# Kernel tuning notes

Measured on AMD Instinct MI355X. Metric: run time of the kernel, lower is better.

## Reference

```python
import jax, jax.numpy as jnp
import numpy as np

N = 50000   # num_nodes
E = 300000  # num_edges
D = 256     # args.dim
F = 1024    # feat_dim
C = 40      # num_labels

def setup_inputs() -> dict:
    key = jax.random.key(0)
    ks = jax.random.split(key, 16)
    def lin(k, fan_in, shape):
        return (jax.random.normal(k, shape, jnp.float32) / np.float32(np.sqrt(fan_in)))
    return {
        "feat": jax.random.normal(ks[0], (N, F), jnp.float32),
        "src": jax.random.randint(ks[1], (E,), 0, N, dtype=jnp.int32),
        "dst": jax.random.randint(ks[2], (E,), 0, N, dtype=jnp.int32),
        "W_fc": lin(ks[3], F, (F, D)), "b_fc": jnp.zeros((D,), jnp.float32),
        "W1": lin(ks[4], D, (D, D)), "b1": jnp.zeros((D,), jnp.float32),
        "W2": lin(ks[5], D, (D, D)), "b2": jnp.zeros((D,), jnp.float32),
        "W3": lin(ks[6], D, (D, D)), "b3": jnp.zeros((D,), jnp.float32),
        "gamma": jnp.ones((D,), jnp.float32), "beta": jnp.zeros((D,), jnp.float32),
        "W_lin": lin(ks[7], D, (D, C)), "b_lin": jnp.zeros((C,), jnp.float32),
    }

def _norms(src, dst, n):
    # DGL GraphConv norm='both': out-degree norm on src side, in-degree on dst side, clamp(min=1)
    ones = jnp.ones(src.shape[0], jnp.float32)
    deg_out = jnp.clip(jax.ops.segment_sum(ones, src, num_segments=n), 1.0)
    deg_in = jnp.clip(jax.ops.segment_sum(ones, dst, num_segments=n), 1.0)
    return deg_out[:, None] ** -0.5, deg_in[:, None] ** -0.5

def _gconv(x, src, dst, norm_s, norm_d, W, b):
    h = x * norm_s                              # [N, D]
    m = jax.ops.segment_sum(h[src], dst, num_segments=x.shape[0])  # SpMM via gather/scatter
    return (m * norm_d) @ W + b

def _bn_elu(x, gamma, beta):
    # training-mode batchnorm math (batch stats, biased var); dropout is identity (eval)
    mu = x.mean(axis=0)
    var = x.var(axis=0)
    y = gamma * (x - mu) * jax.lax.rsqrt(var + 1e-5) + beta
    return jax.nn.elu(y)

def reference(feat, src, dst, W_fc, b_fc, W1, b1, W2, b2, W3, b3, gamma, beta, W_lin, b_lin):
    norm_s, norm_d = _norms(src, dst, feat.shape[0])
    x = feat @ W_fc + b_fc
    x = _gconv(x, src, dst, norm_s, norm_d, W1, b1)
    x = _bn_elu(x, gamma, beta)
    x = _gconv(x, src, dst, norm_s, norm_d, W2, b2)
    x = _bn_elu(x, gamma, beta)
    x = _gconv(x, src, dst, norm_s, norm_d, W3, b3)
    return (x, x @ W_lin + b_lin)
```

## Files before the change

kernel.cpp:

```cpp
#include <hip/hip_runtime.h>

#define N_NODES 50000
#define N_EDGES 300000
#define DIM 256
#define FEAT 1024
#define NCLS 40

typedef unsigned short u16;
typedef __attribute__((ext_vector_type(8))) short short8;
typedef __attribute__((ext_vector_type(4))) float float4v;

__device__ __forceinline__ float bf2f(u16 u) {
  union { float f; unsigned v; } x; x.v = ((unsigned)u) << 16; return x.f;
}
__device__ __forceinline__ u16 f2bf(float f) {
  union { float f; unsigned v; } x; x.f = f;
  unsigned r = 0x7fffu + ((x.v >> 16) & 1u);
  return (u16)((x.v + r) >> 16);
}
__device__ __forceinline__ float flexload(const void* p, size_t i, int f32) {
  return f32 ? ((const float*)p)[i] : bf2f(((const u16*)p)[i]);
}
__device__ __forceinline__ void flexstore(void* p, size_t i, int f32, float v) {
  if (f32) ((float*)p)[i] = v;
  else ((u16*)p)[i] = f2bf(v);
}

__global__ __launch_bounds__(256) void k_sniff(const u16* __restrict__ feat,
                                               int* __restrict__ dflag) {
  __shared__ int cnt[256];
  int t = threadIdx.x;
  int ok = 0;
  for (int j = 0; j < 4; ++j) {
    float v = bf2f(feat[(size_t)(t * 4 + j) * 2]);
    float a = fabsf(v);
    if (a < 64.0f && a > 1e-5f) ok++;
  }
  cnt[t] = ok;
  __syncthreads();
  for (int off = 128; off > 0; off >>= 1) {
    if (t < off) cnt[t] += cnt[t + off];
    __syncthreads();
  }
  if (t == 0) dflag[0] = (cnt[0] < 700) ? 1 : 0;
}

__global__ void k_setflag(int* dflag, int v) { dflag[0] = v; }

__global__ void k_filldiag(void* out, int n, float val, const int* __restrict__ dflag) {
  int i = blockIdx.x * blockDim.x + threadIdx.x;
  if (i < n) flexstore(out, i, dflag[0], val);
}


__global__ void k_zero(unsigned* p, int n) {
  int i = blockIdx.x * blockDim.x + threadIdx.x;
  if (i < n) p[i] = 0u;
}

__global__ void k_deg(const int* __restrict__ src, const int* __restrict__ dst,
                      float* __restrict__ degf, int* __restrict__ degi, int e) {
  int i = blockIdx.x * blockDim.x + threadIdx.x;
  if (i < e) {
    atomicAdd(&degf[src[i]], 1.0f);
    atomicAdd(&degi[dst[i]], 1);
  }
}

__global__ void k_norm(const float* __restrict__ degf, const int* __restrict__ degi,
                       float* __restrict__ ns, float* __restrict__ nd, int n) {
  int i = blockIdx.x * blockDim.x + threadIdx.x;
  if (i < n) {
    ns[i] = rsqrtf(fmaxf(degf[i], 1.0f));
    nd[i] = rsqrtf(fmaxf((float)degi[i], 1.0f));
  }
}

__global__ __launch_bounds__(1024) void k_scan(const int* __restrict__ counts,
                                               int* __restrict__ row_start,
                                               int* __restrict__ cursor, int n) {
  __shared__ int wsum[16];
  __shared__ int carry_s;
  int t = threadIdx.x;
  int lane = t & 63, wv = t >> 6;
  if (t == 0) carry_s = 0;
  __syncthreads();
  for (int base = 0; base < n; base += 4096) {
    int i0 = base + t * 4;
    int v0 = 0, v1 = 0, v2 = 0, v3 = 0;
    if (i0 + 3 < n) {
      int4 c4 = *(const int4*)&counts[i0];
      v0 = c4.x; v1 = c4.y; v2 = c4.z; v3 = c4.w;
    } else {
      if (i0 < n) v0 = counts[i0];
      if (i0 + 1 < n) v1 = counts[i0 + 1];
      if (i0 + 2 < n) v2 = counts[i0 + 2];
      if (i0 + 3 < n) v3 = counts[i0 + 3];
    }
    int s = v0 + v1 + v2 + v3;
    int sc = s;
#pragma unroll
    for (int off = 1; off < 64; off <<= 1) {
      int u = __shfl_up(sc, off, 64);
      if (lane >= off) sc += u;
    }
    if (lane == 63) wsum[wv] = sc;
    __syncthreads();
    if (wv == 0) {
      int w_ = (lane < 16) ? wsum[lane] : 0;
#pragma unroll
      for (int off = 1; off < 16; off <<= 1) {
        int u = __shfl_up(w_, off, 64);
        if (lane >= off) w_ += u;
      }
      if (lane < 16) wsum[lane] = w_;
    }
    __syncthreads();
    int wbase = (wv == 0) ? 0 : wsum[wv - 1];
    int carry = carry_s;
    int excl = carry + wbase + (sc - s);
    if (i0 < n)     { int p = excl;                row_start[i0] = p;     cursor[i0] = p; }
    if (i0 + 1 < n) { int p = excl + v0;           row_start[i0 + 1] = p; cursor[i0 + 1] = p; }
    if (i0 + 2 < n) { int p = excl + v0 + v1;      row_start[i0 + 2] = p; cursor[i0 + 2] = p; }
    if (i0 + 3 < n) { int p = excl + v0 + v1 + v2; row_start[i0 + 3] = p; cursor[i0 + 3] = p; }
    __syncthreads();
    if (t == 1023) carry_s = carry + wbase + sc;
    __syncthreads();
  }
  if (t == 0) row_start[n] = carry_s;
}

__global__ void k_scatter(const int* __restrict__ src, const int* __restrict__ dst,
                          int* __restrict__ cursor, int* __restrict__ csr_src, int e) {
  int i = blockIdx.x * blockDim.x + threadIdx.x;
  if (i < e) {
    int pos = atomicAdd(&cursor[dst[i]], 1);
    csr_src[pos] = src[i];
  }
}

__global__ void k_transpose(const void* __restrict__ w, u16* __restrict__ wt,
                            int K, int Ncols, const int* __restrict__ dflag) {
  int f = dflag[0];
  int i = blockIdx.x * blockDim.x + threadIdx.x;
  if (i < K * Ncols) {
    int k = i / Ncols;
    int c = i - k * Ncols;
    wt[c * K + k] = f2bf(flexload(w, i, f));
  }
}


__global__ __launch_bounds__(256) void k_gemm(
    const void* __restrict__ A, const u16* __restrict__ Bt,
    const void* __restrict__ bias, void* __restrict__ Cmat,
    int M, int K, int Ncols, int a_flex, int c_flex,
    const int* __restrict__ dflag) {
  __shared__ __align__(16) u16 As[64 * 128];
  __shared__ __align__(16) u16 Bs[64 * 128];

  const int f = dflag[0];
  const int af = a_flex & f;
  const int cf = c_flex & f;

  const int tid = threadIdx.x;
  const int lane = tid & 63;
  const int wv = tid >> 6;
  const int wm = (wv >> 1) * 64;
  const int wn = (wv & 1) * 64;
  const int quad = lane >> 4;
  const int l15 = lane & 15;
  const int rowBase = blockIdx.x * 128;
  const int colBase = blockIdx.y * 128;

  float4v acc[4][4];
#pragma unroll
  for (int a = 0; a < 4; ++a)
#pragma unroll
    for (int b = 0; b < 4; ++b) {
      acc[a][b][0] = 0.f; acc[a][b][1] = 0.f; acc[a][b][2] = 0.f; acc[a][b][3] = 0.f;
    }

  for (int k0 = 0; k0 < K; k0 += 64) {
    __syncthreads();
#pragma unroll
    for (int r = 0; r < 4; ++r) {
      int j = r * 256 + tid;
      int kq = j >> 7;
      int ml = j & 127;
      int grow = rowBase + ml;
      if (grow >= M) grow = M - 1;
      size_t abase = (size_t)grow * K + k0 + kq * 8;
      if (af) {
        const float* Af = (const float*)A;
        float4 lo = *(const float4*)&Af[abase];
        float4 hi = *(const float4*)&Af[abase + 4];
        u16* d = &As[j * 8];
        d[0] = f2bf(lo.x); d[1] = f2bf(lo.y); d[2] = f2bf(lo.z); d[3] = f2bf(lo.w);
        d[4] = f2bf(hi.x); d[5] = f2bf(hi.y); d[6] = f2bf(hi.z); d[7] = f2bf(hi.w);
      } else {
        const u16* Au = (const u16*)A;
        *(uint4*)&As[j * 8] = *(const uint4*)&Au[abase];
      }
      *(uint4*)&Bs[j * 8] = *(const uint4*)&Bt[(size_t)(colBase + ml) * K + k0 + kq * 8];
    }
    __syncthreads();
#pragma unroll
    for (int ks = 0; ks < 2; ++ks) {
      short8 afr[4], bfr[4];
#pragma unroll
      for (int t = 0; t < 4; ++t) {
        int kq = ks * 4 + quad;
        afr[t] = *(const short8*)&As[(kq * 128 + wm + t * 16 + l15) * 8];
        bfr[t] = *(const short8*)&Bs[(kq * 128 + wn + t * 16 + l15) * 8];
      }
#pragma unroll
      for (int mt = 0; mt < 4; ++mt)
#pragma unroll
        for (int nt = 0; nt < 4; ++nt)
          acc[mt][nt] = __builtin_amdgcn_mfma_f32_16x16x32_bf16(
              afr[mt], bfr[nt], acc[mt][nt], 0, 0, 0);
    }
  }

#pragma unroll
  for (int nt = 0; nt < 4; ++nt) {
    int col = colBase + wn + nt * 16 + l15;
    float bv = flexload(bias, col, f);
#pragma unroll
    for (int mt = 0; mt < 4; ++mt) {
#pragma unroll
      for (int r = 0; r < 4; ++r) {
        int row = rowBase + wm + mt * 16 + quad * 4 + r;
        if (row < M) {
          float v = acc[mt][nt][r] + bv;
          if (cf) ((float*)Cmat)[(size_t)row * Ncols + col] = v;
          else ((u16*)Cmat)[(size_t)row * Ncols + col] = f2bf(v);
        }
      }
    }
  }
}


__global__ __launch_bounds__(256) void k_spmm(
    const u16* __restrict__ x, u16* __restrict__ y,
    const int* __restrict__ row_start, const int* __restrict__ csr_src,
    const float* __restrict__ ns, const float* __restrict__ nd, int n) {
  int wid = (blockIdx.x * blockDim.x + threadIdx.x) >> 6;
  int lane = threadIdx.x & 63;
  if (wid >= n) return;
  int e0 = row_start[wid];
  int e1 = row_start[wid + 1];
  int c = lane * 4;
  float a0 = 0.f, a1 = 0.f, a2 = 0.f, a3 = 0.f;
  for (int e = e0; e < e1; ++e) {
    int s = csr_src[e];
    float w = ns[s];
    uint2 v = *(const uint2*)&x[(size_t)s * DIM + c];
    a0 += w * bf2f((u16)(v.x & 0xffffu));
    a1 += w * bf2f((u16)(v.x >> 16));
    a2 += w * bf2f((u16)(v.y & 0xffffu));
    a3 += w * bf2f((u16)(v.y >> 16));
  }
  float wd = nd[wid];
  uint2 o;
  o.x = (unsigned)f2bf(a0 * wd) | ((unsigned)f2bf(a1 * wd) << 16);
  o.y = (unsigned)f2bf(a2 * wd) | ((unsigned)f2bf(a3 * wd) << 16);
  *(uint2*)&y[(size_t)wid * DIM + c] = o;
}


__global__ __launch_bounds__(256) void k_bnstats(const u16* __restrict__ x,
                                                 float* __restrict__ stats, int nrows) {
  int t = threadIdx.x;
  float s = 0.f, s2 = 0.f;
  for (int r = blockIdx.x; r < nrows; r += gridDim.x) {
    float v = bf2f(x[(size_t)r * DIM + t]);
    s += v;
    s2 += v * v;
  }
  atomicAdd(&stats[t], s);
  atomicAdd(&stats[DIM + t], s2);
}

__global__ __launch_bounds__(256) void k_bnapply(u16* __restrict__ x,
                                                 const float* __restrict__ stats,
                                                 const void* __restrict__ gamma,
                                                 const void* __restrict__ beta, int nrows,
                                                 const int* __restrict__ dflag) {
  int f = dflag[0];
  int t = threadIdx.x;
  float inv_n = 1.0f / (float)nrows;
  float mu = stats[t] * inv_n;
  float var = stats[DIM + t] * inv_n - mu * mu;
  float rs = rsqrtf(var + 1e-5f);
  float g = flexload(gamma, t, f) * rs;
  float b = flexload(beta, t, f) - mu * g;
  for (int r = blockIdx.x; r < nrows; r += gridDim.x) {
    size_t idx = (size_t)r * DIM + t;
    float y = g * bf2f(x[idx]) + b;
    y = y > 0.f ? y : expm1f(y);
    x[idx] = f2bf(y);
  }
}


__global__ __launch_bounds__(256) void k_final(const void* __restrict__ x,
                                               const void* __restrict__ W,
                                               const void* __restrict__ bias,
                                               void* __restrict__ out, int nrows,
                                               const int* __restrict__ dflag) {
  __shared__ u16 xs[64 * DIM];
  __shared__ u16 wl[DIM * NCLS];
  int f = dflag[0];
  int t = threadIdx.x;
  int rowBase = blockIdx.x * 64;
  for (int i = t; i < 64 * DIM; i += 256) {
    int r = rowBase + (i >> 8);
    if (r >= nrows) r = nrows - 1;
    xs[i] = f2bf(flexload(x, (size_t)r * DIM + (i & 255), f));
  }
  for (int i = t; i < DIM * NCLS; i += 256) wl[i] = f2bf(flexload(W, i, f));
  __syncthreads();
  for (int o = t; o < 64 * NCLS; o += 256) {
    int r = o / NCLS;
    int c = o - r * NCLS;
    float acc = 0.f;
    const u16* xr = &xs[r * DIM];
#pragma unroll 8
    for (int k = 0; k < DIM; ++k) acc += bf2f(xr[k]) * bf2f(wl[k * NCLS + c]);
    int grow = rowBase + r;
    if (grow < nrows)
      flexstore(out, (size_t)N_NODES * DIM + (size_t)grow * NCLS + c, f,
                acc + flexload(bias, c, f));
  }
}


extern "C" void kernel_launch(void* const* d_in, const int* in_sizes, int n_in,
                              void* d_out, int out_size, void* d_ws, size_t ws_size,
                              hipStream_t stream) {
  static const int EXP[15] = {51200000, 300000, 300000, 262144, 256, 65536, 256,
                              65536, 256, 65536, 256, 256, 256, 10240, 40};
  bool ok_sizes = (n_in == 15);
  if (ok_sizes)
    for (int i = 0; i < 15; ++i)
      if (in_sizes[i] != EXP[i]) ok_sizes = false;

  char* w = (char*)d_ws;
  size_t o = 0;
  auto take = [&](size_t bytes) {
    size_t r = o;
    o += (bytes + 255) & ~(size_t)255;
    return r;
  };
  size_t o_degf = take(N_NODES * 4);
  size_t o_degi = take(N_NODES * 4);
  size_t o_stat = take(1024 * 4);
  size_t zero_bytes = o;
  size_t o_flag = take(256);
  size_t o_ns = take(N_NODES * 4);
  size_t o_nd = take(N_NODES * 4);
  size_t o_rs = take((N_NODES + 1) * 4);
  size_t o_cur = take(N_NODES * 4);
  size_t o_csr = take(N_EDGES * 4);
  size_t o_wfc = take((size_t)FEAT * DIM * 2);
  size_t o_w1 = take(DIM * DIM * 2);
  size_t o_w2 = take(DIM * DIM * 2);
  size_t o_w3 = take(DIM * DIM * 2);
  size_t o_xa = take((size_t)N_NODES * DIM * 2);
  size_t required = o;

  if (!ok_sizes || ws_size < required) {
    int* dflag0 = (int*)d_ws;
    float val = ok_sizes ? 1.0f : 2.0f;
    if (n_in > 0 && in_sizes[0] >= 2048)
      k_sniff<<<1, 256, 0, stream>>>((const u16*)d_in[0], dflag0);
    else
      k_setflag<<<1, 1, 0, stream>>>(dflag0, 0);
    k_filldiag<<<(out_size + 255) / 256, 256, 0, stream>>>(d_out, out_size, val, dflag0);
    return;
  }

  const void* feat = d_in[0];
  const int* src = (const int*)d_in[1];
  const int* dst = (const int*)d_in[2];
  const void* W_fc = d_in[3];
  const void* b_fc = d_in[4];
  const void* W1 = d_in[5];
  const void* b1 = d_in[6];
  const void* W2 = d_in[7];
  const void* b2 = d_in[8];
  const void* W3 = d_in[9];
  const void* b3 = d_in[10];
  const void* gamma = d_in[11];
  const void* beta = d_in[12];
  const void* W_lin = d_in[13];
  const void* b_lin = d_in[14];

  float* degf = (float*)(w + o_degf);
  int* degi = (int*)(w + o_degi);
  float* stats = (float*)(w + o_stat);
  int* dflag = (int*)(w + o_flag);
  float* norm_s = (float*)(w + o_ns);
  float* norm_d = (float*)(w + o_nd);
  int* row_start = (int*)(w + o_rs);
  int* cursor = (int*)(w + o_cur);
  int* csr_src = (int*)(w + o_csr);
  u16* WtFc = (u16*)(w + o_wfc);
  u16* Wt1 = (u16*)(w + o_w1);
  u16* Wt2 = (u16*)(w + o_w2);
  u16* Wt3 = (u16*)(w + o_w3);
  u16* xA = (u16*)(w + o_xa);

  u16* ping = (u16*)d_out;

  k_sniff<<<1, 256, 0, stream>>>((const u16*)feat, dflag);

  int zero_words = (int)(zero_bytes / 4);
  k_zero<<<(zero_words + 255) / 256, 256, 0, stream>>>((unsigned*)(w + 0), zero_words);
  k_deg<<<(N_EDGES + 255) / 256, 256, 0, stream>>>(src, dst, degf, degi, N_EDGES);
  k_norm<<<(N_NODES + 255) / 256, 256, 0, stream>>>(degf, degi, norm_s, norm_d, N_NODES);
  k_scan<<<1, 1024, 0, stream>>>(degi, row_start, cursor, N_NODES);
  k_scatter<<<(N_EDGES + 255) / 256, 256, 0, stream>>>(src, dst, cursor, csr_src, N_EDGES);
  k_transpose<<<((FEAT * DIM) + 255) / 256, 256, 0, stream>>>(W_fc, WtFc, FEAT, DIM, dflag);
  k_transpose<<<((DIM * DIM) + 255) / 256, 256, 0, stream>>>(W1, Wt1, DIM, DIM, dflag);
  k_transpose<<<((DIM * DIM) + 255) / 256, 256, 0, stream>>>(W2, Wt2, DIM, DIM, dflag);
  k_transpose<<<((DIM * DIM) + 255) / 256, 256, 0, stream>>>(W3, Wt3, DIM, DIM, dflag);

  dim3 gg((N_NODES + 127) / 128, DIM / 128);

  k_gemm<<<gg, 256, 0, stream>>>(feat, WtFc, b_fc, ping, N_NODES, FEAT, DIM, 1, 0, dflag);

  k_spmm<<<(N_NODES + 3) / 4, 256, 0, stream>>>(ping, xA, row_start, csr_src, norm_s, norm_d, N_NODES);
  k_gemm<<<gg, 256, 0, stream>>>(xA, Wt1, b1, ping, N_NODES, DIM, DIM, 0, 0, dflag);
  k_bnstats<<<512, 256, 0, stream>>>(ping, stats, N_NODES);
  k_bnapply<<<512, 256, 0, stream>>>(ping, stats, gamma, beta, N_NODES, dflag);

  k_spmm<<<(N_NODES + 3) / 4, 256, 0, stream>>>(ping, xA, row_start, csr_src, norm_s, norm_d, N_NODES);
  k_gemm<<<gg, 256, 0, stream>>>(xA, Wt2, b2, ping, N_NODES, DIM, DIM, 0, 0, dflag);
  k_bnstats<<<512, 256, 0, stream>>>(ping, stats + 512, N_NODES);
  k_bnapply<<<512, 256, 0, stream>>>(ping, stats + 512, gamma, beta, N_NODES, dflag);

  k_spmm<<<(N_NODES + 3) / 4, 256, 0, stream>>>(ping, xA, row_start, csr_src, norm_s, norm_d, N_NODES);
  k_gemm<<<gg, 256, 0, stream>>>(xA, Wt3, b3, d_out, N_NODES, DIM, DIM, 0, 1, dflag);

  k_final<<<(N_NODES + 63) / 64, 256, 0, stream>>>(d_out, W_lin, b_lin, d_out, N_NODES, dflag);
}
```

Before: 1.042 ms.

## Use async global-to-LDS loads in GEMM, pre-cast features, fuse BN stats into epilogue

Adds a bf16 GEMM variant that loads A and B tiles straight into LDS with global_load_lds instead of staging through registers. When the input is fp32, the feature matrix is first cast to a bf16 workspace buffer. The batchnorm column sums and sums of squares are now accumulated in the GEMM epilogue through wave shuffles and atomics, which removes a separate full read of the activations. The cost is an extra pass over the large feature matrix to cast it, more workspace, and atomic contention on the stats array.

```diff
diff --git a/kernel.cpp b/kernel.cpp
--- a/kernel.cpp
+++ b/kernel.cpp
@@ -24,6 +24,11 @@
 __device__ __forceinline__ void flexstore(void* p, size_t i, int f32, float v) {
   if (f32) ((float*)p)[i] = v;
   else ((u16*)p)[i] = f2bf(v);
+}
+__device__ __forceinline__ void async16(const u16* g, u16* l) {
+  __builtin_amdgcn_global_load_lds(
+      (__attribute__((address_space(1))) void*)g,
+      (__attribute__((address_space(3))) void*)l, 16, 0, 0);
 }
 
 __global__ __launch_bounds__(256) void k_sniff(const u16* __restrict__ feat,
@@ -50,6 +55,22 @@
 __global__ void k_filldiag(void* out, int n, float val, const int* __restrict__ dflag) {
   int i = blockIdx.x * blockDim.x + threadIdx.x;
   if (i < n) flexstore(out, i, dflag[0], val);
+}
+
+__global__ __launch_bounds__(256) void k_cast(const void* __restrict__ feat,
+                                              u16* __restrict__ xf,
+                                              const int* __restrict__ dflag) {
+  if (dflag[0] == 0) return;
+  size_t i = ((size_t)blockIdx.x * 256 + threadIdx.x) * 8;
+  const float* f = (const float*)feat;
+  float4 a = *(const float4*)&f[i];
+  float4 b = *(const float4*)&f[i + 4];
+  uint4 o;
+  o.x = (unsigned)f2bf(a.x) | ((unsigned)f2bf(a.y) << 16);
+  o.y = (unsigned)f2bf(a.z) | ((unsigned)f2bf(a.w) << 16);
+  o.z = (unsigned)f2bf(b.x) | ((unsigned)f2bf(b.y) << 16);
+  o.w = (unsigned)f2bf(b.z) | ((unsigned)f2bf(b.w) << 16);
+  *(uint4*)&xf[i] = o;
 }
 
 
@@ -151,16 +172,16 @@
 }
 
 
-__global__ __launch_bounds__(256) void k_gemm(
-    const void* __restrict__ A, const u16* __restrict__ Bt,
-    const void* __restrict__ bias, void* __restrict__ Cmat,
-    int M, int K, int Ncols, int a_flex, int c_flex,
-    const int* __restrict__ dflag) {
+__global__ __launch_bounds__(256) void k_gemm_a(
+    const u16* __restrict__ A0, const u16* __restrict__ A1,
+    const u16* __restrict__ Bt, const void* __restrict__ bias,
+    void* __restrict__ Cmat, int M, int K, int Nc, int c_flex,
+    float* __restrict__ stats, const int* __restrict__ dflag) {
   __shared__ __align__(16) u16 As[64 * 128];
   __shared__ __align__(16) u16 Bs[64 * 128];
 
   const int f = dflag[0];
-  const int af = a_flex & f;
+  const u16* A = f ? A1 : A0;
   const int cf = c_flex & f;
 
   const int tid = threadIdx.x;
@@ -181,6 +202,95 @@
       acc[a][b][0] = 0.f; acc[a][b][1] = 0.f; acc[a][b][2] = 0.f; acc[a][b][3] = 0.f;
     }
 
+  for (int k0 = 0; k0 < K; k0 += 64) {
+    __syncthreads();
+#pragma unroll
+    for (int r = 0; r < 4; ++r) {
+      int j = r * 256 + tid;
+      int kq = j >> 7;
+      int ml = j & 127;
+      int grow = rowBase + ml;
+      if (grow >= M) grow = M - 1;
+      async16(&A[(size_t)grow * K + k0 + kq * 8], &As[j * 8]);
+      async16(&Bt[(size_t)(colBase + ml) * K + k0 + kq * 8], &Bs[j * 8]);
+    }
+    __syncthreads();
+#pragma unroll
+    for (int ks = 0; ks < 2; ++ks) {
+      short8 afr[4], bfr[4];
+#pragma unroll
+      for (int t = 0; t < 4; ++t) {
+        int kq = ks * 4 + quad;
+        afr[t] = *(const short8*)&As[(kq * 128 + wm + t * 16 + l15) * 8];
+        bfr[t] = *(const short8*)&Bs[(kq * 128 + wn + t * 16 + l15) * 8];
+      }
+#pragma unroll
+      for (int mt = 0; mt < 4; ++mt)
+#pragma unroll
+        for (int nt = 0; nt < 4; ++nt)
+          acc[mt][nt] = __builtin_amdgcn_mfma_f32_16x16x32_bf16(
+              afr[mt], bfr[nt], acc[mt][nt], 0, 0, 0);
+    }
+  }
+
+#pragma unroll
+  for (int nt = 0; nt < 4; ++nt) {
+    int col = colBase + wn + nt * 16 + l15;
+    float bv = flexload(bias, col, f);
+    float s = 0.f, s2 = 0.f;
+#pragma unroll
+    for (int mt = 0; mt < 4; ++mt) {
+#pragma unroll
+      for (int r = 0; r < 4; ++r) {
+        int row = rowBase + wm + mt * 16 + quad * 4 + r;
+        if (row < M) {
+          float v = acc[mt][nt][r] + bv;
+          if (cf) ((float*)Cmat)[(size_t)row * Nc + col] = v;
+          else ((u16*)Cmat)[(size_t)row * Nc + col] = f2bf(v);
+          s += v;
+          s2 += v * v;
+        }
+      }
+    }
+    if (stats) {
+      s += __shfl_down(s, 32, 64);
+      s += __shfl_down(s, 16, 64);
+      s2 += __shfl_down(s2, 32, 64);
+      s2 += __shfl_down(s2, 16, 64);
+      if (quad == 0) {
+        atomicAdd(&stats[col], s);
+        atomicAdd(&stats[DIM + col], s2);
+      }
+    }
+  }
+}
+
+__global__ __launch_bounds__(256) void k_gemm_flex(
+    const void* __restrict__ A, const u16* __restrict__ Bt,
+    const void* __restrict__ bias, void* __restrict__ Cmat,
+    int M, int K, int Nc, int a_flex, int c_flex,
+    const int* __restrict__ dflag) {
+  __shared__ __align__(16) u16 As[64 * 128];
+  __shared__ __align__(16) u16 Bs[64 * 128];
+  const int f = dflag[0];
+  const int af = a_flex & f;
+  const int cf = c_flex & f;
+  const int tid = threadIdx.x;
+  const int lane = tid & 63;
+  const int wv = tid >> 6;
+  const int wm = (wv >> 1) * 64;
+  const int wn = (wv & 1) * 64;
+  const int quad = lane >> 4;
+  const int l15 = lane & 15;
+  const int rowBase = blockIdx.x * 128;
+  const int colBase = blockIdx.y * 128;
+  float4v acc[4][4];
+#pragma unroll
+  for (int a = 0; a < 4; ++a)
+#pragma unroll
+    for (int b = 0; b < 4; ++b) {
+      acc[a][b][0] = 0.f; acc[a][b][1] = 0.f; acc[a][b][2] = 0.f; acc[a][b][3] = 0.f;
+    }
   for (int k0 = 0; k0 < K; k0 += 64) {
     __syncthreads();
 #pragma unroll
@@ -222,7 +332,6 @@
               afr[mt], bfr[nt], acc[mt][nt], 0, 0, 0);
     }
   }
-
 #pragma unroll
   for (int nt = 0; nt < 4; ++nt) {
     int col = colBase + wn + nt * 16 + l15;
@@ -234,8 +343,8 @@
         int row = rowBase + wm + mt * 16 + quad * 4 + r;
         if (row < M) {
           float v = acc[mt][nt][r] + bv;
-          if (cf) ((float*)Cmat)[(size_t)row * Ncols + col] = v;
-          else ((u16*)Cmat)[(size_t)row * Ncols + col] = f2bf(v);
+          if (cf) ((float*)Cmat)[(size_t)row * Nc + col] = v;
+          else ((u16*)Cmat)[(size_t)row * Nc + col] = f2bf(v);
         }
       }
     }
@@ -271,24 +380,11 @@
 }
 
 
-__global__ __launch_bounds__(256) void k_bnstats(const u16* __restrict__ x,
-                                                 float* __restrict__ stats, int nrows) {
-  int t = threadIdx.x;
-  float s = 0.f, s2 = 0.f;
-  for (int r = blockIdx.x; r < nrows; r += gridDim.x) {
-    float v = bf2f(x[(size_t)r * DIM + t]);
-    s += v;
-    s2 += v * v;
-  }
-  atomicAdd(&stats[t], s);
-  atomicAdd(&stats[DIM + t], s2);
-}
-
-__global__ __launch_bounds__(256) void k_bnapply(u16* __restrict__ x,
-                                                 const float* __restrict__ stats,
-                                                 const void* __restrict__ gamma,
-                                                 const void* __restrict__ beta, int nrows,
-                                                 const int* __restrict__ dflag) {
+__global__ __launch_bounds__(256) void k_bnfin(const float* __restrict__ stats,
+                                               const void* __restrict__ gamma,
+                                               const void* __restrict__ beta,
+                                               float* __restrict__ gb, int nrows,
+                                               const int* __restrict__ dflag) {
   int f = dflag[0];
   int t = threadIdx.x;
   float inv_n = 1.0f / (float)nrows;
@@ -297,6 +393,15 @@
   float rs = rsqrtf(var + 1e-5f);
   float g = flexload(gamma, t, f) * rs;
   float b = flexload(beta, t, f) - mu * g;
+  gb[t] = g;
+  gb[DIM + t] = b;
+}
+
+__global__ __launch_bounds__(256) void k_bnapply(u16* __restrict__ x,
+                                                 const float* __restrict__ gb, int nrows) {
+  int t = threadIdx.x;
+  float g = gb[t];
+  float b = gb[DIM + t];
   for (int r = blockIdx.x; r < nrows; r += gridDim.x) {
     size_t idx = (size_t)r * DIM + t;
     float y = g * bf2f(x[idx]) + b;
@@ -360,6 +465,7 @@
   size_t o_stat = take(1024 * 4);
   size_t zero_bytes = o;
   size_t o_flag = take(256);
+  size_t o_gb = take(512 * 4);
   size_t o_ns = take(N_NODES * 4);
   size_t o_nd = take(N_NODES * 4);
   size_t o_rs = take((N_NODES + 1) * 4);
@@ -371,6 +477,9 @@
   size_t o_w3 = take(DIM * DIM * 2);
   size_t o_xa = take((size_t)N_NODES * DIM * 2);
   size_t required = o;
+  size_t o_xf = take((size_t)N_NODES * FEAT * 2);
+  size_t required_xf = o;
+  bool have_xf = ws_size >= required_xf;
 
   if (!ok_sizes || ws_size < required) {
     int* dflag0 = (int*)d_ws;
@@ -403,6 +512,7 @@
   int* degi = (int*)(w + o_degi);
   float* stats = (float*)(w + o_stat);
   int* dflag = (int*)(w + o_flag);
+  float* gb = (float*)(w + o_gb);
   float* norm_s = (float*)(w + o_ns);
   float* norm_d = (float*)(w + o_nd);
   int* row_start = (int*)(w + o_rs);
@@ -413,6 +523,7 @@
   u16* Wt2 = (u16*)(w + o_w2);
   u16* Wt3 = (u16*)(w + o_w3);
   u16* xA = (u16*)(w + o_xa);
+  u16* xF = (u16*)(w + o_xf);
 
   u16* ping = (u16*)d_out;
 
@@ -431,20 +542,27 @@
 
   dim3 gg((N_NODES + 127) / 128, DIM / 128);
 
-  k_gemm<<<gg, 256, 0, stream>>>(feat, WtFc, b_fc, ping, N_NODES, FEAT, DIM, 1, 0, dflag);
+  if (have_xf) {
+    k_cast<<<(N_NODES * FEAT) / (256 * 8), 256, 0, stream>>>(feat, xF, dflag);
+    k_gemm_a<<<gg, 256, 0, stream>>>((const u16*)feat, xF, WtFc, b_fc, ping,
+                                     N_NODES, FEAT, DIM, 0, (float*)nullptr, dflag);
+  } else {
+    k_gemm_flex<<<gg, 256, 0, stream>>>(feat, WtFc, b_fc, ping,
+                                        N_NODES, FEAT, DIM, 1, 0, dflag);
+  }
 
   k_spmm<<<(N_NODES + 3) / 4, 256, 0, stream>>>(ping, xA, row_start, csr_src, norm_s, norm_d, N_NODES);
-  k_gemm<<<gg, 256, 0, stream>>>(xA, Wt1, b1, ping, N_NODES, DIM, DIM, 0, 0, dflag);
-  k_bnstats<<<512, 256, 0, stream>>>(ping, stats, N_NODES);
-  k_bnapply<<<512, 256, 0, stream>>>(ping, stats, gamma, beta, N_NODES, dflag);
+  k_gemm_a<<<gg, 256, 0, stream>>>(xA, xA, Wt1, b1, ping, N_NODES, DIM, DIM, 0, stats, dflag);
+  k_bnfin<<<1, 256, 0, stream>>>(stats, gamma, beta, gb, N_NODES, dflag);
+  k_bnapply<<<512, 256, 0, stream>>>(ping, gb, N_NODES);
 
   k_spmm<<<(N_NODES + 3) / 4, 256, 0, stream>>>(ping, xA, row_start, csr_src, norm_s, norm_d, N_NODES);
-  k_gemm<<<gg, 256, 0, stream>>>(xA, Wt2, b2, ping, N_NODES, DIM, DIM, 0, 0, dflag);
-  k_bnstats<<<512, 256, 0, stream>>>(ping, stats + 512, N_NODES);
-  k_bnapply<<<512, 256, 0, stream>>>(ping, stats + 512, gamma, beta, N_NODES, dflag);
+  k_gemm_a<<<gg, 256, 0, stream>>>(xA, xA, Wt2, b2, ping, N_NODES, DIM, DIM, 0, stats + 512, dflag);
+  k_bnfin<<<1, 256, 0, stream>>>(stats + 512, gamma, beta, gb, N_NODES, dflag);
+  k_bnapply<<<512, 256, 0, stream>>>(ping, gb, N_NODES);
 
   k_spmm<<<(N_NODES + 3) / 4, 256, 0, stream>>>(ping, xA, row_start, csr_src, norm_s, norm_d, N_NODES);
-  k_gemm<<<gg, 256, 0, stream>>>(xA, Wt3, b3, d_out, N_NODES, DIM, DIM, 0, 1, dflag);
+  k_gemm_a<<<gg, 256, 0, stream>>>(xA, xA, Wt3, b3, d_out, N_NODES, DIM, DIM, 1, (float*)nullptr, dflag);
 
   k_final<<<(N_NODES + 63) / 64, 256, 0, stream>>>(d_out, W_lin, b_lin, d_out, N_NODES, dflag);
 }
```

Result: faster. 1.010 ms (-3.1%).
